# Kernel optimization log

Measured on AMD Instinct MI355X. Metric: run time of the kernel, lower is better.

The kernel has to match this reference:

```python
import jax, jax.numpy as jnp
import numpy as np

B, K, H, W = 16, 32, 28, 28   # batch, set size, image h, image w
HID, OUT = 64, 64             # hid_dim, out_dim
NOPS = 8                      # permutation-equivariant 3->3 pool/broadcast basis ops


def setup_inputs() -> dict:
    key = jax.random.key(0)
    ks = jax.random.split(key, 8)
    def p(k, shape, fan_in):
        return jax.random.normal(k, shape, jnp.float32) / np.float32(np.sqrt(fan_in))
    return dict(
        x=jax.random.normal(ks[0], (B, K, H, W), jnp.float32),
        conv1_w=p(ks[1], (32, 1, 3, 3), 9),
        conv1_b=jnp.zeros((32,), jnp.float32),
        conv2_w=p(ks[2], (64, 32, 3, 3), 32 * 9),
        conv2_b=jnp.zeros((64,), jnp.float32),
        fc_w=p(ks[3], (HID, 64 * 7 * 7), 64 * 7 * 7),
        fc_b=jnp.zeros((HID,), jnp.float32),
        eq_w=p(ks[4], (HID, OUT, NOPS), HID * NOPS),
        eq_b=jnp.zeros((OUT,), jnp.float32),
        out_w=p(ks[5], (1, OUT), OUT),
        out_b=jnp.zeros((1,), jnp.float32),
    )


def _conv2d(x, w, b):
    y = jax.lax.conv_general_dilated(x, w, (1, 1), 'SAME',
                                     dimension_numbers=('NCHW', 'OIHW', 'NCHW'))
    return y + b[None, :, None, None]


def _maxpool2(x):
    return jax.lax.reduce_window(x, -jnp.inf, jax.lax.max,
                                 (1, 1, 2, 2), (1, 1, 2, 2), 'VALID')


def _forward(x, conv1_w, conv1_b, conv2_w, conv2_b, fc_w, fc_b, eq_w, eq_b, out_w, out_b):
    # --- BasicConvNet embed: (B*K, 1, H, W) -> (B*K, HID) ---
    x1 = x.reshape(B * K, 1, H, W)
    h1 = _maxpool2(jax.nn.relu(_conv2d(x1, conv1_w, conv1_b)))   # (B*K, 32, 14, 14)
    h2 = _maxpool2(jax.nn.relu(_conv2d(h1, conv2_w, conv2_b)))   # (B*K, 64, 7, 7)
    feat = jax.nn.relu(h2.reshape(B * K, -1) @ fc_w.T + fc_b)    # (B*K, HID)
    x4 = feat.reshape(B, K, HID)

    # --- triple outer product: (B, HID, K, K, K), no contracted index ---
    x5 = jnp.einsum('bid,bjd,bkd->bdijk', x4, x4, x4)

    # --- SetEq3to3: 8 equivariant pool/broadcast basis ops, contracted with eq_w[d,e,o].
    # Contract each pooled tensor with its slice of eq_w BEFORE broadcasting (same math,
    # avoids materializing 8 full (B,d,K,K,K) op tensors). ---
    m_i  = x5.mean(2)           # (B, d, j, k)
    m_j  = x5.mean(3)           # (B, d, i, k)
    m_k  = x5.mean(4)           # (B, d, i, j)
    m_ij = m_i.mean(2)          # (B, d, k)
    m_ik = m_i.mean(3)          # (B, d, j)
    m_jk = m_j.mean(3)          # (B, d, i)
    m_all = m_ij.mean(2)        # (B, d)

    x6 = (jnp.einsum('bdijk,de->beijk', x5, eq_w[:, :, 0])
          + jnp.einsum('bdjk,de->bejk', m_i, eq_w[:, :, 1])[:, :, None, :, :]
          + jnp.einsum('bdik,de->beik', m_j, eq_w[:, :, 2])[:, :, :, None, :]
          + jnp.einsum('bdij,de->beij', m_k, eq_w[:, :, 3])[:, :, :, :, None]
          + jnp.einsum('bdk,de->bek', m_ij, eq_w[:, :, 4])[:, :, None, None, :]
          + jnp.einsum('bdj,de->bej', m_ik, eq_w[:, :, 5])[:, :, None, :, None]
          + jnp.einsum('bdi,de->bei', m_jk, eq_w[:, :, 6])[:, :, :, None, None]
          + jnp.einsum('bd,de->be', m_all, eq_w[:, :, 7])[:, :, None, None, None]
          + eq_b[None, :, None, None, None])          # (B, OUT, K, K, K)

    # permute to channels-last, relu, pool over (i,j,k), relu, final linear
    x7 = jax.nn.relu(x6.transpose(0, 2, 3, 4, 1))     # (B, K, K, K, OUT)
    x8 = x7.mean(axis=(1, 2, 3))                      # (B, OUT)
    x9 = jax.nn.relu(x8)
    # dropout_prob = 0 -> identity
    return x9 @ out_w.T + out_b                       # (B, 1)


def reference(x, conv1_w, conv1_b, conv2_w, conv2_b, fc_w, fc_b, eq_w, eq_b, out_w, out_b):
    return _forward(x, conv1_w, conv1_b, conv2_w, conv2_b, fc_w, fc_b,
                    eq_w, eq_b, out_w, out_b)
```

## Files before the change

kernel.cpp:

```cpp
#include <hip/hip_runtime.h>
#include <hip/hip_bf16.h>


typedef __attribute__((ext_vector_type(8))) short short8;
typedef __attribute__((ext_vector_type(4))) float f32x4;

__device__ __forceinline__ f32x4 mfma_bf16(short8 a, short8 b, f32x4 c) {
  return __builtin_amdgcn_mfma_f32_16x16x32_bf16(a, b, c, 0, 0, 0);
}

__device__ __forceinline__ unsigned short f2bs(float f) {
  unsigned int u = __float_as_uint(f);
  unsigned int r = u + 0x7fffu + ((u >> 16) & 1u);
  return (unsigned short)(r >> 16);
}
__device__ __forceinline__ unsigned int pk2(float x, float y) {
  union { __hip_bfloat162 h; unsigned int u; } cv;
  cv.h = __float22bfloat162_rn(make_float2(x, y));
  return cv.u;
}
__device__ __forceinline__ void ub8(const short* p, float* f) {
  uint4 u = *(const uint4*)p;
  f[0] = __uint_as_float(u.x << 16); f[1] = __uint_as_float(u.x & 0xffff0000u);
  f[2] = __uint_as_float(u.y << 16); f[3] = __uint_as_float(u.y & 0xffff0000u);
  f[4] = __uint_as_float(u.z << 16); f[5] = __uint_as_float(u.z & 0xffff0000u);
  f[6] = __uint_as_float(u.w << 16); f[7] = __uint_as_float(u.w & 0xffff0000u);
}

__global__ __launch_bounds__(256, 2) void k12_conv(const float* __restrict__ x,
    const float* __restrict__ w1, const float* __restrict__ b1,
    const float* __restrict__ w2, const float* __restrict__ b2,
    short* __restrict__ h2b,
    const float* __restrict__ eqw, float* __restrict__ W7t, short* __restrict__ Wtb,
    const float* __restrict__ fcw, short* __restrict__ fcwb) {
  const int n = blockIdx.x, t = threadIdx.x;
  if (n >= 512) {
    if (n < 520) {
      const int m = n - 512;
      for (int idx = t; idx < 4096; idx += 256) {
        int e = idx >> 6, d = idx & 63;
        float v = eqw[d*512 + e*8 + m];
        if (m == 7) W7t[idx] = v;
        else        Wtb[m*4096 + idx] = (short)f2bs(v);
      }
    } else {
      int base = (n - 520)*12544 + t;
      for (int q = 0; q < 49; ++q) {
        int idx = base + q*256;
        fcwb[idx] = (short)f2bs(fcw[idx]);
      }
    }
    return;
  }
  __shared__ float si[30*30];
  __shared__ float sw[32*9];
  __shared__ float sb[32];
  __shared__ __align__(16) short inT[16*18*40];
  const int wv = t >> 6, l = t & 63, quad = l >> 4, col = l & 15;

  const int c_out = wv*16 + col;
  float w72[72];
  {
    const float4* src = (const float4*)(w2 + c_out*288 + quad*72);
#pragma unroll
    for (int q = 0; q < 18; ++q) {
      float4 v = src[q];
      w72[q*4+0] = v.x; w72[q*4+1] = v.y; w72[q*4+2] = v.z; w72[q*4+3] = v.w;
    }
  }
  union SU { short8 v; unsigned int u[4]; };
  short8 Bq[9];
#pragma unroll
  for (int dd = 0; dd < 9; ++dd) {
    SU b;
#pragma unroll
    for (int q = 0; q < 4; ++q)
      b.u[q] = pk2(w72[(2*q)*9 + dd], w72[(2*q+1)*9 + dd]);
    Bq[dd] = b.v;
  }
  const float bb2 = b2[c_out];

  for (int idx = t; idx < 900; idx += 256) si[idx] = 0.f;
  {
    unsigned int* zp = (unsigned int*)inT;
    for (int idx = t; idx < 5760; idx += 256) zp[idx] = 0u;
  }
  for (int idx = t; idx < 288; idx += 256) sw[idx] = w1[idx];
  if (t < 32) sb[t] = b1[t];
  __syncthreads();
  for (int idx = t; idx < 784; idx += 256) {
    int y = idx / 28, xx = idx - y*28;
    si[(y+1)*30 + xx + 1] = x[n*784 + idx];
  }
  __syncthreads();

  {
    const int cg = t & 7;
    float wreg[4][9], breg[4];
#pragma unroll
    for (int cc = 0; cc < 4; ++cc) {
      breg[cc] = sb[cg*4 + cc];
#pragma unroll
      for (int q = 0; q < 9; ++q) wreg[cc][q] = sw[(cg*4 + cc)*9 + q];
    }
    for (int idx = t; idx < 1568; idx += 256) {
      int pos = idx >> 3;
      int py = pos / 14, px = pos - py*14;
      float pt[4][4];
#pragma unroll
      for (int r = 0; r < 4; ++r)
#pragma unroll
        for (int q = 0; q < 4; ++q)
          pt[r][q] = si[(2*py + r)*30 + 2*px + q];
      float res[4];
#pragma unroll
      for (int cc = 0; cc < 4; ++cc) {
        float best = 0.f;
#pragma unroll
        for (int a = 0; a < 2; ++a)
#pragma unroll
          for (int b3 = 0; b3 < 2; ++b3) {
            float v = breg[cc]
              + wreg[cc][0]*pt[a+0][b3+0] + wreg[cc][1]*pt[a+0][b3+1] + wreg[cc][2]*pt[a+0][b3+2]
              + wreg[cc][3]*pt[a+1][b3+0] + wreg[cc][4]*pt[a+1][b3+1] + wreg[cc][5]*pt[a+1][b3+2]
              + wreg[cc][6]*pt[a+2][b3+0] + wreg[cc][7]*pt[a+2][b3+1] + wreg[cc][8]*pt[a+2][b3+2];
            best = fmaxf(best, v);
          }
        res[cc] = best;
      }
      uint2 pkd;
      pkd.x = pk2(res[0], res[1]);
      pkd.y = pk2(res[2], res[3]);
      *(uint2*)&inT[(py+1)*720 + (px+1)*40 + cg*4] = pkd;
    }
  }
  __syncthreads();

  for (int p = 0; p < 7; ++p) {
    short8 Ar[4][3];
#pragma unroll
    for (int rr = 0; rr < 4; ++rr)
#pragma unroll
      for (int dx = 0; dx < 3; ++dx)
        Ar[rr][dx] = *(const short8*)&inT[(2*p + rr)*720 + (col + dx)*40 + quad*8];
    f32x4 a0 = {0.f,0.f,0.f,0.f}, a1 = {0.f,0.f,0.f,0.f};
#pragma unroll
    for (int dy = 0; dy < 3; ++dy)
#pragma unroll
      for (int dx = 0; dx < 3; ++dx) {
        a0 = mfma_bf16(Ar[dy][dx],     Bq[dy*3 + dx], a0);
        a1 = mfma_bf16(Ar[dy + 1][dx], Bq[dy*3 + dx], a1);
      }
#pragma unroll
    for (int a = 0; a < 2; ++a) {
      int px = quad*2 + a;
      if (px < 7) {
        float m0 = fmaxf(fmaxf(a0[2*a], a0[2*a + 1]), fmaxf(a1[2*a], a1[2*a + 1]));
        h2b[n*3136 + c_out*49 + p*7 + px] = (short)f2bs(fmaxf(m0 + bb2, 0.f));
      }
    }
  }
}

__global__ __launch_bounds__(256) void k3_mfma(const short* __restrict__ h2b,
    const short* __restrict__ fcwb, float* __restrict__ part) {
  const int blk = blockIdx.x, kp = blockIdx.y, t = threadIdx.x;
  const int w = t >> 6, l = t & 63, quad = l >> 4, col = l & 15;
  const int mt = w & 1, nh = w >> 1;
  const int img = blk*32 + mt*16 + col;
  const short* Ap = h2b + img*3136 + kp*224 + quad*8;
  const short* B0 = fcwb + (nh*32 + col)*3136 + kp*224 + quad*8;
  const short* B1 = fcwb + (nh*32 + 16 + col)*3136 + kp*224 + quad*8;
  f32x4 acc0 = {0.f,0.f,0.f,0.f}, acc1 = {0.f,0.f,0.f,0.f};
#pragma unroll
  for (int q = 0; q < 7; ++q) {
    short8 A  = *(const short8*)(Ap + q*32);
    short8 b0 = *(const short8*)(B0 + q*32);
    short8 b1 = *(const short8*)(B1 + q*32);
    acc0 = mfma_bf16(A, b0, acc0);
    acc1 = mfma_bf16(A, b1, acc1);
  }
  const int e0 = nh*32 + col, e1 = e0 + 16;
  const int base = blk*32 + mt*16 + quad*4;
  float* dst = part + kp*32768;
#pragma unroll
  for (int r = 0; r < 4; ++r) {
    dst[(base + r)*64 + e0] = acc0[r];
    dst[(base + r)*64 + e1] = acc1[r];
  }
}

__global__ __launch_bounds__(256) void k4_prep(const float* __restrict__ part,
    const float* __restrict__ fb, const float* __restrict__ W7t,
    const float* __restrict__ eqb, float* __restrict__ feat,
    float* __restrict__ s, float* __restrict__ t7c) {
  __shared__ __align__(16) float sf[2048];
  __shared__ float ss[64];
  const int b = blockIdx.x, t = threadIdx.x;
  for (int v4 = t; v4 < 512; v4 += 256) {
    float4 a = {0.f, 0.f, 0.f, 0.f};
#pragma unroll
    for (int kp = 0; kp < 14; ++kp) {
      float4 p = *(const float4*)&part[kp*32768 + b*2048 + v4*4];
      a.x += p.x; a.y += p.y; a.z += p.z; a.w += p.w;
    }
    float4 fbv = *(const float4*)&fb[(v4*4) & 63];
    float4 r;
    r.x = fmaxf(a.x + fbv.x, 0.f);
    r.y = fmaxf(a.y + fbv.y, 0.f);
    r.z = fmaxf(a.z + fbv.z, 0.f);
    r.w = fmaxf(a.w + fbv.w, 0.f);
    *(float4*)&sf[v4*4] = r;
    *(float4*)&feat[b*2048 + v4*4] = r;
  }
  __syncthreads();
  if (t < 64) {
    float a = 0.f;
    for (int i = 0; i < 32; ++i) a += sf[i*64 + t];
    a *= (1.f/32.f);
    s[b*64 + t] = a;
    ss[t] = a;
  }
  __syncthreads();
  if (t < 64) {
    const float* W7 = W7t + t*64;
    float t7 = 0.f;
    for (int d = 0; d < 64; ++d) {
      float sv = ss[d];
      t7 += sv*sv*sv * W7[d];
    }
    t7c[b*64 + t] = t7 + eqb[t];
  }
}

__global__ __launch_bounds__(256, 2) void k5_mfma(const float* __restrict__ feat,
    const float* __restrict__ s_, const short* __restrict__ Wtb,
    const float* __restrict__ t7c, float* __restrict__ x8p) {
  __shared__ __align__(16) float Fm[32*68];
  __shared__ __align__(16) float FI[64];
  __shared__ __align__(16) float SV[64];
  __shared__ __align__(16) float C0[64];
  __shared__ float C0P[128];
  __shared__ __align__(16) float KCt[64*36];
  __shared__ float JCf[32*68];
  __shared__ float RED[256];
  __shared__ __align__(16) short Fb[32*72];
  __shared__ __align__(16) short QPb[64*72];
  __shared__ __align__(16) short Gbuf[9216];

  const int i = blockIdx.x, b = blockIdx.y, t = threadIdx.x;
  const int w = t >> 6, l = t & 63, quad = l >> 4, col = l & 15;
  short* G2b = Gbuf;
  short* G3b = Gbuf + 4608;
  short* PTt = Gbuf;

  for (int idx = t; idx < 2048; idx += 256) {
    int r = idx >> 6, d = idx & 63;
    float v = feat[b*2048 + idx];
    Fm[r*68 + d] = v;
    Fb[r*72 + d] = (short)f2bs(v);
  }
  if (t < 64) { FI[t] = feat[b*2048 + i*64 + t]; SV[t] = s_[b*64 + t]; }
  __syncthreads();

  {
    const int e = t >> 2, dbase = (t & 3) * 16;
#pragma unroll
    for (int h = 0; h < 2; ++h) {
      int off = dbase + h*8;
      float w0[8], w1[8], w2[8], w3[8], w4[8], w5[8];
      ub8(&Wtb[0*4096 + e*64 + off], w0);
      ub8(&Wtb[1*4096 + e*64 + off], w1);
      ub8(&Wtb[2*4096 + e*64 + off], w2);
      ub8(&Wtb[3*4096 + e*64 + off], w3);
      ub8(&Wtb[4*4096 + e*64 + off], w4);
      ub8(&Wtb[5*4096 + e*64 + off], w5);
      uint4 qv, g2v, g3v;
      unsigned int* qp = &qv.x;
      unsigned int* g2p = &g2v.x;
      unsigned int* g3p = &g3v.x;
#pragma unroll
      for (int j = 0; j < 4; ++j) {
        float fi0 = FI[off + 2*j],     fi1 = FI[off + 2*j + 1];
        float s0  = SV[off + 2*j],     s1  = SV[off + 2*j + 1];
        float q0 = fi0*w0[2*j]   + s0*w1[2*j];
        float q1 = fi1*w0[2*j+1] + s1*w1[2*j+1];
        float a0 = s0*(fi0*w2[2*j]   + s0*w4[2*j]);
        float a1 = s1*(fi1*w2[2*j+1] + s1*w4[2*j+1]);
        float c0 = s0*(fi0*w3[2*j]   + s0*w5[2*j]);
        float c1 = s1*(fi1*w3[2*j+1] + s1*w5[2*j+1]);
        qp[j]  = pk2(q0, q1);
        g2p[j] = pk2(a0, a1);
        g3p[j] = pk2(c0, c1);
      }
      *(uint4*)&QPb[e*72 + off] = qv;
      *(uint4*)&G2b[e*72 + off] = g2v;
      *(uint4*)&G3b[e*72 + off] = g3v;
    }
  }
  if (t < 128) {
    int e = t & 63, dh = t >> 6;
    const short* W6 = Wtb + 6*4096 + e*64 + dh*32;
    float a = 0.f;
#pragma unroll
    for (int g = 0; g < 4; ++g) {
      float wf[8];
      ub8(&W6[g*8], wf);
#pragma unroll
      for (int dd = 0; dd < 8; ++dd) {
        int d = dh*32 + g*8 + dd;
        float sd = SV[d];
        a += sd*sd*FI[d]*wf[dd];
      }
    }
    C0P[dh*64 + e] = a;
  }
  __syncthreads();

  if (w < 2) {
    const short* G = w ? G3b : G2b;
    short8 Bf[4][2];
#pragma unroll
    for (int n = 0; n < 4; ++n)
#pragma unroll
      for (int s2 = 0; s2 < 2; ++s2)
        Bf[n][s2] = *(const short8*)&G[(n*16 + col)*72 + s2*32 + quad*8];
#pragma unroll
    for (int m = 0; m < 2; ++m) {
      short8 A0 = *(const short8*)&Fb[(m*16 + col)*72 + quad*8];
      short8 A1 = *(const short8*)&Fb[(m*16 + col)*72 + 32 + quad*8];
#pragma unroll
      for (int n = 0; n < 4; ++n) {
        f32x4 z = {0.f, 0.f, 0.f, 0.f};
        f32x4 ac = mfma_bf16(A1, Bf[n][1], mfma_bf16(A0, Bf[n][0], z));
        if (w == 0) {
#pragma unroll
          for (int r = 0; r < 4; ++r)
            KCt[(n*16 + col)*36 + m*16 + quad*4 + r] = ac[r];
        } else {
#pragma unroll
          for (int r = 0; r < 4; ++r)
            JCf[(m*16 + quad*4 + r)*68 + n*16 + col] = ac[r];
        }
      }
    }
  } else if (w == 2) {
    C0[l] = C0P[l] + C0P[64 + l] + t7c[b*64 + l];
  }
  __syncthreads();

  float c0v[4];
#pragma unroll
  for (int n = 0; n < 4; ++n) c0v[n] = C0[n*16 + col];
  short8 Bq[4][2];
#pragma unroll
  for (int n = 0; n < 4; ++n)
#pragma unroll
    for (int s2 = 0; s2 < 2; ++s2)
      Bq[n][s2] = *(const short8*)&QPb[(n*16 + col)*72 + s2*32 + quad*8];
  float sum[4] = {0.f, 0.f, 0.f, 0.f};

  for (int g = 0; g < 8; ++g) {
    for (int lin = t; lin < 2048; lin += 256) {
      int row = lin >> 4, dg = lin & 15;
      int jr = g*4 + (row >> 5);
      int kr = row & 31;
      float4 fa = *(const float4*)&Fm[jr*68 + dg*4];
      float4 fbv = *(const float4*)&Fm[kr*68 + dg*4];
      uint2 p;
      p.x = pk2(fa.x*fbv.x, fa.y*fbv.y);
      p.y = pk2(fa.z*fbv.z, fa.w*fbv.w);
      *(uint2*)&PTt[row*72 + dg*4] = p;
    }
    __syncthreads();
#pragma unroll
    for (int u = 0; u < 2; ++u) {
      const int mtl = w*2 + u;
      const int j = g*4 + (mtl >> 1);
      const int kb2 = mtl & 1;
      short8 A0 = *(const short8*)&PTt[(mtl*16 + col)*72 + quad*8];
      short8 A1 = *(const short8*)&PTt[(mtl*16 + col)*72 + 32 + quad*8];
      float jc[4];
#pragma unroll
      for (int n = 0; n < 4; ++n) jc[n] = JCf[j*68 + n*16 + col] + c0v[n];
#pragma unroll
      for (int n = 0; n < 4; ++n) {
        f32x4 z = {0.f, 0.f, 0.f, 0.f};
        f32x4 ac = mfma_bf16(A1, Bq[n][1], mfma_bf16(A0, Bq[n][0], z));
        float4 kc = *(const float4*)&KCt[(n*16 + col)*36 + kb2*16 + quad*4];
        sum[n] += fmaxf(ac[0] + kc.x + jc[n], 0.f);
        sum[n] += fmaxf(ac[1] + kc.y + jc[n], 0.f);
        sum[n] += fmaxf(ac[2] + kc.z + jc[n], 0.f);
        sum[n] += fmaxf(ac[3] + kc.w + jc[n], 0.f);
      }
    }
    __syncthreads();
  }

#pragma unroll
  for (int n = 0; n < 4; ++n) {
    float v = sum[n];
    v += __shfl_xor(v, 16, 64);
    v += __shfl_xor(v, 32, 64);
    if (l < 16) RED[w*64 + n*16 + l] = v;
  }
  __syncthreads();
  if (t < 64) {
    float tot = RED[t] + RED[64 + t] + RED[128 + t] + RED[192 + t];
    x8p[(b*32 + i)*64 + t] = tot;
  }
}

__global__ __launch_bounds__(64) void k6_out(const float* __restrict__ x8p,
    const float* __restrict__ ow, const float* __restrict__ ob,
    float* __restrict__ out) {
  const int bb = blockIdx.x, t = threadIdx.x;
  float a = 0.f;
#pragma unroll
  for (int i = 0; i < 32; ++i) a += x8p[(bb*32 + i)*64 + t];
  float v = fmaxf(a * (1.f/32768.f), 0.f) * ow[t];
#pragma unroll
  for (int off = 32; off > 0; off >>= 1) v += __shfl_down(v, off, 64);
  if (t == 0) out[bb] = v + ob[0];
}

extern "C" void kernel_launch(void* const* d_in, const int* in_sizes, int n_in,
                              void* d_out, int out_size, void* d_ws, size_t ws_size,
                              hipStream_t stream) {
  const float* x   = (const float*)d_in[0];
  const float* c1w = (const float*)d_in[1];
  const float* c1b = (const float*)d_in[2];
  const float* c2w = (const float*)d_in[3];
  const float* c2b = (const float*)d_in[4];
  const float* fcw = (const float*)d_in[5];
  const float* fcb = (const float*)d_in[6];
  const float* eqw = (const float*)d_in[7];
  const float* eqb = (const float*)d_in[8];
  const float* ow  = (const float*)d_in[9];
  const float* ob  = (const float*)d_in[10];
  float* out = (float*)d_out;

  short* h2b  = (short*)d_ws;
  float* feat = (float*)(h2b + 512*3136);
  float* s    = feat + 32768;
  float* t7c  = s + 1024;
  float* x8p  = t7c + 1024;
  float* W7t  = x8p + 32768;
  short* Wtb  = (short*)(W7t + 4096);
  short* fcwb = Wtb + 7*4096;
  float* part = (float*)(fcwb + 200704);

  hipLaunchKernelGGL(k12_conv, dim3(536), dim3(256), 0, stream,
                     x, c1w, c1b, c2w, c2b, h2b, eqw, W7t, Wtb, fcw, fcwb);
  hipLaunchKernelGGL(k3_mfma,  dim3(16, 14), dim3(256), 0, stream, h2b, fcwb, part);
  hipLaunchKernelGGL(k4_prep,  dim3(16),  dim3(256), 0, stream,
                     part, fcb, W7t, eqb, feat, s, t7c);
  hipLaunchKernelGGL(k5_mfma,  dim3(32, 16), dim3(256), 0, stream, feat, s, Wtb, t7c, x8p);
  hipLaunchKernelGGL(k6_out,   dim3(16),  dim3(64),  0, stream, x8p, ow, ob, out);
}
```

Baseline: 124.4 us.

## Split k5 into a precompute kernel and a main MFMA kernel via global memory

The fused k5 kernel is split in two. The first kernel computes per-(b,i) QP, KC, JC and C0 tensors and writes them to a global workspace. The second loads them back into shared memory and runs the main triple-product MFMA loop, and the per-iteration barrier moves to the top of the loop. This lowers per-kernel shared memory and register pressure, which may raise occupancy, at the cost of an extra launch and roughly 12 MB of global traffic.

```diff
diff --git a/kernel.cpp b/kernel.cpp
--- a/kernel.cpp
+++ b/kernel.cpp
@@ -233,32 +233,24 @@
   }
 }
 
-__global__ __launch_bounds__(256, 2) void k5_mfma(const float* __restrict__ feat,
+__global__ __launch_bounds__(256, 2) void k5a_pre(const float* __restrict__ feat,
     const float* __restrict__ s_, const short* __restrict__ Wtb,
-    const float* __restrict__ t7c, float* __restrict__ x8p) {
-  __shared__ __align__(16) float Fm[32*68];
-  __shared__ __align__(16) float FI[64];
-  __shared__ __align__(16) float SV[64];
-  __shared__ __align__(16) float C0[64];
+    const float* __restrict__ t7c, short* __restrict__ qpg,
+    float* __restrict__ kcg, float* __restrict__ jcg, float* __restrict__ c0g) {
+  __shared__ __align__(16) short Fb[32*72];
+  __shared__ __align__(16) short G2b[64*72];
+  __shared__ __align__(16) short G3b[64*72];
+  __shared__ float FI[64];
+  __shared__ float SV[64];
   __shared__ float C0P[128];
-  __shared__ __align__(16) float KCt[64*36];
-  __shared__ float JCf[32*68];
-  __shared__ float RED[256];
-  __shared__ __align__(16) short Fb[32*72];
-  __shared__ __align__(16) short QPb[64*72];
-  __shared__ __align__(16) short Gbuf[9216];
 
   const int i = blockIdx.x, b = blockIdx.y, t = threadIdx.x;
   const int w = t >> 6, l = t & 63, quad = l >> 4, col = l & 15;
-  short* G2b = Gbuf;
-  short* G3b = Gbuf + 4608;
-  short* PTt = Gbuf;
+  const int bi = b*32 + i;
 
   for (int idx = t; idx < 2048; idx += 256) {
     int r = idx >> 6, d = idx & 63;
-    float v = feat[b*2048 + idx];
-    Fm[r*68 + d] = v;
-    Fb[r*72 + d] = (short)f2bs(v);
+    Fb[r*72 + d] = (short)f2bs(feat[b*2048 + idx]);
   }
   if (t < 64) { FI[t] = feat[b*2048 + i*64 + t]; SV[t] = s_[b*64 + t]; }
   __syncthreads();
@@ -293,7 +285,7 @@
         g2p[j] = pk2(a0, a1);
         g3p[j] = pk2(c0, c1);
       }
-      *(uint4*)&QPb[e*72 + off] = qv;
+      *(uint4*)&qpg[bi*4096 + e*64 + off] = qv;
       *(uint4*)&G2b[e*72 + off] = g2v;
       *(uint4*)&G3b[e*72 + off] = g3v;
     }
@@ -336,17 +328,50 @@
         if (w == 0) {
 #pragma unroll
           for (int r = 0; r < 4; ++r)
-            KCt[(n*16 + col)*36 + m*16 + quad*4 + r] = ac[r];
+            kcg[bi*2048 + (n*16 + col)*32 + m*16 + quad*4 + r] = ac[r];
         } else {
 #pragma unroll
           for (int r = 0; r < 4; ++r)
-            JCf[(m*16 + quad*4 + r)*68 + n*16 + col] = ac[r];
+            jcg[bi*2048 + (m*16 + quad*4 + r)*64 + n*16 + col] = ac[r];
         }
       }
     }
   } else if (w == 2) {
-    C0[l] = C0P[l] + C0P[64 + l] + t7c[b*64 + l];
-  }
+    c0g[bi*64 + l] = C0P[l] + C0P[64 + l] + t7c[b*64 + l];
+  }
+}
+
+__global__ __launch_bounds__(256, 2) void k5b_main(const float* __restrict__ feat,
+    const short* __restrict__ qpg, const float* __restrict__ kcg,
+    const float* __restrict__ jcg, const float* __restrict__ c0g,
+    float* __restrict__ x8p) {
+  __shared__ __align__(16) float Fm[32*68];
+  __shared__ __align__(16) short QPb[64*72];
+  __shared__ __align__(16) float KCt[64*36];
+  __shared__ float JCf[32*68];
+  __shared__ float C0[64];
+  __shared__ float RED[256];
+  __shared__ __align__(16) short PTt[9216];
+
+  const int i = blockIdx.x, b = blockIdx.y, t = threadIdx.x;
+  const int w = t >> 6, l = t & 63, quad = l >> 4, col = l & 15;
+  const int bi = b*32 + i;
+
+  for (int idx = t; idx < 2048; idx += 256) {
+    int r = idx >> 6, d = idx & 63;
+    Fm[r*68 + d] = feat[b*2048 + idx];
+  }
+  for (int idx = t; idx < 512; idx += 256) {
+    int e = idx >> 3, c8 = (idx & 7) * 8;
+    *(uint4*)&QPb[e*72 + c8] = *(const uint4*)&qpg[bi*4096 + e*64 + c8];
+  }
+  for (int idx = t; idx < 2048; idx += 256) {
+    int e = idx >> 5, k = idx & 31;
+    KCt[e*36 + k] = kcg[bi*2048 + idx];
+    int j = idx >> 6, e2 = idx & 63;
+    JCf[j*68 + e2] = jcg[bi*2048 + idx];
+  }
+  if (t < 64) C0[t] = c0g[bi*64 + t];
   __syncthreads();
 
   float c0v[4];
@@ -361,6 +386,7 @@
   float sum[4] = {0.f, 0.f, 0.f, 0.f};
 
   for (int g = 0; g < 8; ++g) {
+    __syncthreads();
     for (int lin = t; lin < 2048; lin += 256) {
       int row = lin >> 4, dg = lin & 15;
       int jr = g*4 + (row >> 5);
@@ -394,7 +420,6 @@
         sum[n] += fmaxf(ac[3] + kc.w + jc[n], 0.f);
       }
     }
-    __syncthreads();
   }
 
 #pragma unroll
@@ -449,12 +474,19 @@
   short* Wtb  = (short*)(W7t + 4096);
   short* fcwb = Wtb + 7*4096;
   float* part = (float*)(fcwb + 200704);
+  short* qpg  = (short*)(part + 458752);
+  float* kcg  = (float*)(qpg + 512*4096);
+  float* jcg  = kcg + 512*2048;
+  float* c0g  = jcg + 512*2048;
 
   hipLaunchKernelGGL(k12_conv, dim3(536), dim3(256), 0, stream,
                      x, c1w, c1b, c2w, c2b, h2b, eqw, W7t, Wtb, fcw, fcwb);
   hipLaunchKernelGGL(k3_mfma,  dim3(16, 14), dim3(256), 0, stream, h2b, fcwb, part);
   hipLaunchKernelGGL(k4_prep,  dim3(16),  dim3(256), 0, stream,
                      part, fcb, W7t, eqb, feat, s, t7c);
-  hipLaunchKernelGGL(k5_mfma,  dim3(32, 16), dim3(256), 0, stream, feat, s, Wtb, t7c, x8p);
+  hipLaunchKernelGGL(k5a_pre,  dim3(32, 16), dim3(256), 0, stream,
+                     feat, s, Wtb, t7c, qpg, kcg, jcg, c0g);
+  hipLaunchKernelGGL(k5b_main, dim3(32, 16), dim3(256), 0, stream,
+                     feat, qpg, kcg, jcg, c0g, x8p);
   hipLaunchKernelGGL(k6_out,   dim3(16),  dim3(64),  0, stream, x8p, ow, ob, out);
 }
```

After: 134.5 us. 1.08x slower.
